# Kernel optimization log

Hardware: AMD Instinct MI355X
Metric: run time of the kernel (lower is better)

The kernel has to match this reference:

```python
import jax, jax.numpy as jnp
import numpy as np

D = 512          # embedding_dim (cfg.hidden_size)
K = 1024         # codebook_size
DECAY = 0.99
EPS = 1e-05
COMMITMENT_COST = 0.25


def setup_inputs() -> dict:
    key = jax.random.key(0)
    k1, k2, k3 = jax.random.split(key, 3)
    return {
        "inputs": jax.random.normal(k1, (32, 1024, D), dtype=jnp.float32),
        "embedding_weight": jax.random.normal(k2, (K, D), dtype=jnp.float32),
        "ema_cluster_size": jnp.zeros((K,), dtype=jnp.float32),
        "ema_w": jax.random.normal(k3, (K, D), dtype=jnp.float32),
    }


def reference(inputs, embedding_weight, ema_cluster_size, ema_w):
    input_shape = inputs.shape
    flat = inputs.reshape(-1, D)  # [N, D]

    # Squared L2 distances to every codebook entry: [N, K]
    distances = (
        jnp.sum(flat ** 2, axis=1, keepdims=True)
        + jnp.sum(embedding_weight ** 2, axis=1)
        - 2.0 * flat @ embedding_weight.T
    )
    idx = jnp.argmin(distances, axis=1)                      # [N]
    encodings = jax.nn.one_hot(idx, K, dtype=flat.dtype)     # [N, K]

    # ---- EMA codebook update (training path) ----
    counts = jnp.sum(encodings, axis=0)                      # == bincount(idx)
    new_cs = ema_cluster_size * DECAY + (1.0 - DECAY) * counts
    n = jnp.sum(new_cs)
    new_cs = (new_cs + EPS) / (n + K * EPS) * n              # Laplace smoothing
    # dw = encodings.T @ flat, done as a fused gather-reduce instead of dense matmul
    dw = jax.ops.segment_sum(flat, idx, num_segments=K)      # [K, D]
    new_ema_w = ema_w * DECAY + (1.0 - DECAY) * dw
    new_embedding = new_ema_w / new_cs[:, None]              # updated codebook

    # quantized = encodings @ new_embedding, expressed as a gather
    quantized = new_embedding[idx].reshape(input_shape)

    e_latent_loss = jnp.mean((jax.lax.stop_gradient(quantized) - inputs) ** 2)
    loss = COMMITMENT_COST * e_latent_loss

    # straight-through estimator
    quantized = inputs + jax.lax.stop_gradient(quantized - inputs)

    avg_probs = jnp.mean(encodings, axis=0)
    perplexity = jnp.exp(-jnp.sum(avg_probs * jnp.log(avg_probs + 1e-10)))
    return (loss, quantized, perplexity, encodings)
```

## Files before the change

### kernel.cpp

```cpp
#include <hip/hip_runtime.h>

#define NROWS 32768
#define DIM   512
#define KC    1024

typedef __attribute__((ext_vector_type(8)))  short short8v;
typedef __attribute__((ext_vector_type(16))) float f32x16;

#define AS1 __attribute__((address_space(1)))
#define AS3 __attribute__((address_space(3)))

__device__ __forceinline__ void split_bf16(float v, short& hi, short& lo) {
    unsigned u = __float_as_uint(v);
    unsigned r = u + 0x7FFFu + ((u >> 16) & 1u);
    hi = (short)(r >> 16);
    float hif = __uint_as_float(r & 0xFFFF0000u);
    float rem = v - hif;
    unsigned u2 = __float_as_uint(rem);
    unsigned r2 = u2 + 0x7FFFu + ((u2 >> 16) & 1u);
    lo = (short)(r2 >> 16);
}

__device__ __forceinline__ void conv8(const float4 a, const float4 b,
                                      short8v& hi, short8v& lo) {
    short h, l;
    split_bf16(a.x, h, l); hi[0] = h; lo[0] = l;
    split_bf16(a.y, h, l); hi[1] = h; lo[1] = l;
    split_bf16(a.z, h, l); hi[2] = h; lo[2] = l;
    split_bf16(a.w, h, l); hi[3] = h; lo[3] = l;
    split_bf16(b.x, h, l); hi[4] = h; lo[4] = l;
    split_bf16(b.y, h, l); hi[5] = h; lo[5] = l;
    split_bf16(b.z, h, l); hi[6] = h; lo[6] = l;
    split_bf16(b.w, h, l); hi[7] = h; lo[7] = l;
}

__device__ __forceinline__ unsigned long long pack_key(float d, int c) {
    unsigned u = __float_as_uint(d);
    u = (u & 0x80000000u) ? ~u : (u | 0x80000000u);
    return ((unsigned long long)u << 32) | (unsigned)c;
}

__global__ __launch_bounds__(256) void k_eprep(const float* __restrict__ E,
                                               short* __restrict__ efrag,
                                               float* __restrict__ en2,
                                               int* __restrict__ counts,
                                               unsigned long long* __restrict__ packed) {
    __shared__ short hbuf[32][520];
    __shared__ short lbuf[32][520];
    int b = blockIdx.x, t = threadIdx.x;
    const float* src = E + (size_t)b * 32 * DIM;
    short* dst = efrag + (size_t)b * 32768;

    unsigned long long* p = packed + b * 1024;
    #pragma unroll
    for (int i = 0; i < 4; ++i) p[t + i * 256] = 0xFFFFFFFFFFFFFFFFull;
    if (b == 0) {
        #pragma unroll
        for (int i = 0; i < 4; ++i) counts[t + i * 256] = 0;
    }

    #pragma unroll
    for (int f = 0; f < 16; ++f) {
        int u = t + f * 256;
        int row = u >> 7, c4 = (u & 127) * 4;
        float4 v = *reinterpret_cast<const float4*>(&src[row * DIM + c4]);
        short4 h4, l4;
        split_bf16(v.x, h4.x, l4.x); split_bf16(v.y, h4.y, l4.y);
        split_bf16(v.z, h4.z, l4.z); split_bf16(v.w, h4.w, l4.w);
        *reinterpret_cast<short4*>(&hbuf[row][c4]) = h4;
        *reinterpret_cast<short4*>(&lbuf[row][c4]) = l4;
    }
    __syncthreads();
    #pragma unroll
    for (int f = 0; f < 16; ++f) {
        int u = t + f * 256;
        int lane = u & 63, h = (u >> 6) & 1, kb = u >> 7;
        int row = lane & 31, k0 = kb * 16 + (lane >> 5) * 8;
        const short* s = h ? &lbuf[row][k0] : &hbuf[row][k0];
        short8v val = *reinterpret_cast<const short8v*>(s);
        *reinterpret_cast<short8v*>(&dst[(size_t)u * 8]) = val;
    }

    int w = t >> 6, lane = t & 63;
    for (int cc = 0; cc < 8; ++cc) {
        int c = b * 32 + w * 8 + cc;
        const float* row = E + (size_t)c * DIM;
        float4 a = *reinterpret_cast<const float4*>(&row[lane * 8]);
        float4 bb = *reinterpret_cast<const float4*>(&row[lane * 8 + 4]);
        float s = a.x*a.x + a.y*a.y + a.z*a.z + a.w*a.w
                + bb.x*bb.x + bb.y*bb.y + bb.z*bb.z + bb.w*bb.w;
        #pragma unroll
        for (int off = 32; off; off >>= 1) s += __shfl_xor(s, off);
        if (!lane) en2[c] = s;
    }
}

__global__ __launch_bounds__(256, 2) void k_argmin(const float* __restrict__ x,
                                                   const short* __restrict__ efrag,
                                                   const float* __restrict__ en2,
                                                   unsigned long long* __restrict__ packed) {
    __shared__ short sbuf[3][12288];
    const int tid = threadIdx.x;
    const int w = tid >> 6, l = tid & 63;
    const int wr = w >> 1, wc = w & 1;
    const int l31 = l & 31, lh = l >> 5;

    int bid = blockIdx.x;
    int xcd = bid & 7, j = bid >> 3;
    int row0 = (xcd * 32 + (j >> 2)) * 128;
    int c0   = (j & 3) * 256;

    const float* axsrc = x + (size_t)(row0 + w * 32 + l31) * DIM + lh * 8;
    const short* gsrc[4];
    #pragma unroll
    for (int s = 0; s < 4; ++s) {
        int gb = w * 2 + (s >> 1), h = s & 1;
        gsrc[s] = efrag + (size_t)(c0 / 32 + gb) * 32768 + h * 512 + l * 8;
    }

    f32x16 acc[2][4];
    #pragma unroll
    for (int a = 0; a < 2; ++a)
        #pragma unroll
        for (int b = 0; b < 4; ++b)
            #pragma unroll
            for (int r = 0; r < 16; ++r) acc[a][b][r] = 0.f;

    float4 a00 = *reinterpret_cast<const float4*>(axsrc);
    float4 a01 = *reinterpret_cast<const float4*>(axsrc + 4);
    __builtin_amdgcn_sched_barrier(0);
    #pragma unroll
    for (int s = 0; s < 4; ++s)
        __builtin_amdgcn_global_load_lds((const AS1 void*)gsrc[s],
                                         (AS3 void*)&sbuf[0][(8 + w * 4 + s) * 512],
                                         16, 0, 0);
    __builtin_amdgcn_sched_barrier(0);
    float4 a10 = *reinterpret_cast<const float4*>(axsrc + 16);
    float4 a11 = *reinterpret_cast<const float4*>(axsrc + 20);
    __builtin_amdgcn_sched_barrier(0);
    #pragma unroll
    for (int s = 0; s < 4; ++s)
        __builtin_amdgcn_global_load_lds((const AS1 void*)(gsrc[s] + 1024),
                                         (AS3 void*)&sbuf[1][(8 + w * 4 + s) * 512],
                                         16, 0, 0);
    {
        asm volatile("s_waitcnt vmcnt(10)" ::: "memory");
        short8v hi, lo; conv8(a00, a01, hi, lo);
        *reinterpret_cast<short8v*>(&sbuf[0][(w * 2 + 0) * 512 + l * 8]) = hi;
        *reinterpret_cast<short8v*>(&sbuf[0][(w * 2 + 1) * 512 + l * 8]) = lo;
        asm volatile("s_waitcnt vmcnt(4)" ::: "memory");
        conv8(a10, a11, hi, lo);
        *reinterpret_cast<short8v*>(&sbuf[1][(w * 2 + 0) * 512 + l * 8]) = hi;
        *reinterpret_cast<short8v*>(&sbuf[1][(w * 2 + 1) * 512 + l * 8]) = lo;
        asm volatile("s_waitcnt lgkmcnt(0)" ::: "memory");
        __builtin_amdgcn_s_barrier();
    }

    #pragma unroll 3
    for (int kb = 0; kb < 30; ++kb) {
        const int cur = kb % 3, nxt = (kb + 2) % 3;
        float4 an0 = *reinterpret_cast<const float4*>(axsrc + (kb + 2) * 16);
        float4 an1 = *reinterpret_cast<const float4*>(axsrc + (kb + 2) * 16 + 4);
        __builtin_amdgcn_sched_barrier(0);
        #pragma unroll
        for (int s = 0; s < 4; ++s)
            __builtin_amdgcn_global_load_lds(
                (const AS1 void*)(gsrc[s] + (size_t)(kb + 2) * 1024),
                (AS3 void*)&sbuf[nxt][(8 + w * 4 + s) * 512], 16, 0, 0);
        {
            short8v ah[2], al[2], bh[4], bl[4];
            const short* sb = sbuf[cur];
            #pragma unroll
            for (int m = 0; m < 2; ++m) {
                int g = wr * 2 + m;
                ah[m] = *reinterpret_cast<const short8v*>(&sb[(g * 2 + 0) * 512 + l * 8]);
                al[m] = *reinterpret_cast<const short8v*>(&sb[(g * 2 + 1) * 512 + l * 8]);
            }
            #pragma unroll
            for (int n = 0; n < 4; ++n) {
                int g = 4 + wc * 4 + n;
                bh[n] = *reinterpret_cast<const short8v*>(&sb[(g * 2 + 0) * 512 + l * 8]);
                bl[n] = *reinterpret_cast<const short8v*>(&sb[(g * 2 + 1) * 512 + l * 8]);
            }
            #pragma unroll
            for (int m = 0; m < 2; ++m)
                #pragma unroll
                for (int n = 0; n < 4; ++n) {
                    acc[m][n] = __builtin_amdgcn_mfma_f32_32x32x16_bf16(
                        ah[m], bh[n], acc[m][n], 0, 0, 0);
                    acc[m][n] = __builtin_amdgcn_mfma_f32_32x32x16_bf16(
                        ah[m], bl[n], acc[m][n], 0, 0, 0);
                    acc[m][n] = __builtin_amdgcn_mfma_f32_32x32x16_bf16(
                        al[m], bh[n], acc[m][n], 0, 0, 0);
                }
        }
        asm volatile("s_waitcnt vmcnt(4)" ::: "memory");
        {
            short8v hi, lo; conv8(an0, an1, hi, lo);
            *reinterpret_cast<short8v*>(&sbuf[nxt][(w * 2 + 0) * 512 + l * 8]) = hi;
            *reinterpret_cast<short8v*>(&sbuf[nxt][(w * 2 + 1) * 512 + l * 8]) = lo;
        }
        asm volatile("s_waitcnt lgkmcnt(0)" ::: "memory");
        __builtin_amdgcn_s_barrier();
    }

    #pragma unroll
    for (int e = 0; e < 2; ++e) {
        const int kb = 30 + e, cur = kb % 3;
        short8v ah[2], al[2], bh[4], bl[4];
        const short* sb = sbuf[cur];
        #pragma unroll
        for (int m = 0; m < 2; ++m) {
            int g = wr * 2 + m;
            ah[m] = *reinterpret_cast<const short8v*>(&sb[(g * 2 + 0) * 512 + l * 8]);
            al[m] = *reinterpret_cast<const short8v*>(&sb[(g * 2 + 1) * 512 + l * 8]);
        }
        #pragma unroll
        for (int n = 0; n < 4; ++n) {
            int g = 4 + wc * 4 + n;
            bh[n] = *reinterpret_cast<const short8v*>(&sb[(g * 2 + 0) * 512 + l * 8]);
            bl[n] = *reinterpret_cast<const short8v*>(&sb[(g * 2 + 1) * 512 + l * 8]);
        }
        #pragma unroll
        for (int m = 0; m < 2; ++m)
            #pragma unroll
            for (int n = 0; n < 4; ++n) {
                acc[m][n] = __builtin_amdgcn_mfma_f32_32x32x16_bf16(
                    ah[m], bh[n], acc[m][n], 0, 0, 0);
                acc[m][n] = __builtin_amdgcn_mfma_f32_32x32x16_bf16(
                    ah[m], bl[n], acc[m][n], 0, 0, 0);
                acc[m][n] = __builtin_amdgcn_mfma_f32_32x32x16_bf16(
                    al[m], bh[n], acc[m][n], 0, 0, 0);
            }
        if (e == 0) {
            asm volatile("s_waitcnt vmcnt(0) lgkmcnt(0)" ::: "memory");
            __builtin_amdgcn_s_barrier();
        }
    }

    float e2[4];
    #pragma unroll
    for (int n = 0; n < 4; ++n) e2[n] = en2[c0 + wc * 128 + n * 32 + l31];
    #pragma unroll
    for (int m = 0; m < 2; ++m) {
        #pragma unroll
        for (int r = 0; r < 16; ++r) {
            unsigned long long key = 0xFFFFFFFFFFFFFFFFull;
            #pragma unroll
            for (int n = 0; n < 4; ++n) {
                float d = fmaf(-2.f, acc[m][n][r], e2[n]);
                unsigned long long k = pack_key(d, c0 + wc * 128 + n * 32 + l31);
                if (k < key) key = k;
            }
            #pragma unroll
            for (int off = 1; off < 32; off <<= 1) {
                unsigned long long o = __shfl_xor(key, off);
                if (o < key) key = o;
            }
            if (l31 == 0) {
                int grow = row0 + wr * 64 + m * 32 + (r & 3) + 8 * (r >> 2) + 4 * lh;
                atomicMin(&packed[grow], key);
            }
        }
    }
}

__global__ __launch_bounds__(256) void k_hist(const unsigned long long* __restrict__ packed,
                                              int* __restrict__ idx,
                                              int* __restrict__ counts) {
    __shared__ int h[KC];
    for (int i = threadIdx.x; i < KC; i += 256) h[i] = 0;
    __syncthreads();
    int g = blockIdx.x * 256 + threadIdx.x;
    int c = (int)(unsigned)(packed[g] & 0xFFFFFFFFull);
    idx[g] = c;
    atomicAdd(&h[c], 1);
    __syncthreads();
    for (int i = threadIdx.x; i < KC; i += 256)
        if (h[i]) atomicAdd(&counts[i], h[i]);
}

__global__ __launch_bounds__(1024) void k_meta(const int* __restrict__ counts,
                                               const float* __restrict__ ema_cs,
                                               float* __restrict__ smoothed,
                                               int* __restrict__ offsets,
                                               int* __restrict__ cursor,
                                               float* __restrict__ perp_out) {
    __shared__ float ws1[16], ws2[16];
    __shared__ int wsum[16];
    int t = threadIdx.x, lane = t & 63, w = t >> 6;
    int cnt = counts[t];
    float cs = ema_cs[t] * 0.99f + 0.01f * (float)cnt;
    float p = (float)cnt / 32768.f;
    float v1 = cs, v2 = p * logf(p + 1e-10f);
    #pragma unroll
    for (int off = 32; off; off >>= 1) {
        v1 += __shfl_xor(v1, off);
        v2 += __shfl_xor(v2, off);
    }
    int s = cnt;
    #pragma unroll
    for (int off = 1; off < 64; off <<= 1) {
        int u = __shfl_up(s, off);
        if (lane >= off) s += u;
    }
    if (lane == 0) { ws1[w] = v1; ws2[w] = v2; }
    if (lane == 63) wsum[w] = s;
    __syncthreads();
    float n = 0.f;
    #pragma unroll
    for (int i = 0; i < 16; ++i) n += ws1[i];
    smoothed[t] = (cs + 1e-5f) / (n + 1024.f * 1e-5f) * n;
    if (t == 0) {
        float sp = 0.f;
        #pragma unroll
        for (int i = 0; i < 16; ++i) sp += ws2[i];
        perp_out[0] = expf(-sp);
    }
    int wo = 0;
    for (int i = 0; i < 16; ++i) if (i < w) wo += wsum[i];
    int off_ = wo + s - cnt;
    offsets[t] = off_;
    cursor[t] = off_;
}

__global__ __launch_bounds__(256) void k_scatter(const int* __restrict__ idx,
                                                 int* __restrict__ cursor,
                                                 int* __restrict__ bucket) {
    int g = blockIdx.x * 256 + threadIdx.x;
    int c = idx[g];
    int pos = atomicAdd(&cursor[c], 1);
    bucket[pos] = g;
}

__global__ __launch_bounds__(256) void k_dw(const float* __restrict__ x,
                                            const float* __restrict__ ema_w,
                                            const int* __restrict__ offsets,
                                            const int* __restrict__ counts,
                                            const int* __restrict__ bucket,
                                            const float* __restrict__ smoothed,
                                            float* __restrict__ newE) {
    __shared__ int rows[256];
    int k = blockIdx.x >> 1, half = blockIdx.x & 1, t = threadIdx.x;
    int d = half * 256 + t;
    int beg = offsets[k], m = counts[k];
    float a = 0.f;
    for (int base = 0; base < m; base += 256) {
        int n = min(256, m - base);
        __syncthreads();
        if (t < n) rows[t] = bucket[beg + base + t];
        __syncthreads();
        int i = 0;
        for (; i + 4 <= n; i += 4) {
            float v0 = x[(size_t)rows[i]     * DIM + d];
            float v1 = x[(size_t)rows[i + 1] * DIM + d];
            float v2 = x[(size_t)rows[i + 2] * DIM + d];
            float v3 = x[(size_t)rows[i + 3] * DIM + d];
            a += v0 + v1 + v2 + v3;
        }
        for (; i < n; ++i) a += x[(size_t)rows[i] * DIM + d];
    }
    newE[(size_t)k * DIM + d] =
        (ema_w[(size_t)k * DIM + d] * 0.99f + 0.01f * a) / smoothed[k];
}

__global__ __launch_bounds__(256) void k_qe(const float* __restrict__ x,
                                            const int* __restrict__ idx,
                                            const float* __restrict__ newE,
                                            float* __restrict__ outq,
                                            float* __restrict__ enc,
                                            float* __restrict__ partials) {
    int b = blockIdx.x, t = threadIdx.x;
    int row8 = b * 8;
    float lp = 0.f;
    #pragma unroll
    for (int it = 0; it < 4; ++it) {
        int slot = t + it * 256;
        int r = slot >> 7;
        int c4 = (slot & 127) * 4;
        int row = row8 + r;
        int code = idx[row];
        float4 in = *reinterpret_cast<const float4*>(&x[(size_t)row * DIM + c4]);
        float4 q  = *reinterpret_cast<const float4*>(&newE[(size_t)code * DIM + c4]);
        float4 d;
        d.x = q.x - in.x; d.y = q.y - in.y; d.z = q.z - in.z; d.w = q.w - in.w;
        float4 o;
        o.x = in.x + d.x; o.y = in.y + d.y; o.z = in.z + d.z; o.w = in.w + d.w;
        *reinterpret_cast<float4*>(&outq[(size_t)row * DIM + c4]) = o;
        lp += d.x*d.x + d.y*d.y + d.z*d.z + d.w*d.w;
    }
    {
        int er = row8 + (t >> 5);
        int l32 = t & 31;
        int one = idx[er];
        float4* dst = reinterpret_cast<float4*>(enc + (size_t)er * KC);
        #pragma unroll
        for (int s = 0; s < 8; ++s) {
            int c4 = l32 + s * 32;
            int base = c4 * 4;
            float4 v;
            v.x = (one == base)     ? 1.f : 0.f;
            v.y = (one == base + 1) ? 1.f : 0.f;
            v.z = (one == base + 2) ? 1.f : 0.f;
            v.w = (one == base + 3) ? 1.f : 0.f;
            dst[c4] = v;
        }
    }
    #pragma unroll
    for (int off = 32; off; off >>= 1) lp += __shfl_xor(lp, off);
    __shared__ float wr[4];
    int lane = t & 63, w = t >> 6;
    if (!lane) wr[w] = lp;
    __syncthreads();
    if (t == 0) partials[b] = wr[0] + wr[1] + wr[2] + wr[3];
}

__global__ __launch_bounds__(256) void k_lossfin(const float* __restrict__ partials,
                                                 float* __restrict__ out0) {
    __shared__ double red[256];
    double s = 0.0;
    for (int i = threadIdx.x; i < 4096; i += 256) s += (double)partials[i];
    red[threadIdx.x] = s; __syncthreads();
    for (int st = 128; st; st >>= 1) {
        if (threadIdx.x < st) red[threadIdx.x] += red[threadIdx.x + st];
        __syncthreads();
    }
    if (!threadIdx.x) out0[0] = (float)(0.25 * red[0] / 16777216.0);
}

extern "C" void kernel_launch(void* const* d_in, const int* in_sizes, int n_in,
                              void* d_out, int out_size, void* d_ws, size_t ws_size,
                              hipStream_t stream) {
    const float* x   = (const float*)d_in[0];
    const float* E   = (const float*)d_in[1];
    const float* ecs = (const float*)d_in[2];
    const float* emw = (const float*)d_in[3];
    float* out = (float*)d_out;

    char* ws = (char*)d_ws;
    int*   idx      = (int*)(ws + 0);
    int*   bucket   = (int*)(ws + 131072);
    float* en2      = (float*)(ws + 262144);
    int*   counts   = (int*)(ws + 266240);
    int*   offsets  = (int*)(ws + 270336);
    int*   cursor   = (int*)(ws + 274432);
    float* smoothed = (float*)(ws + 278528);
    float* newE     = (float*)(ws + 282624);
    float* partials = (float*)(ws + 282624 + 2097152);
    unsigned long long* packed = (unsigned long long*)newE;

    float* out_loss = out;
    float* out_q    = out + 1;
    float* out_perp = out + 16777217;
    float* out_enc  = out + 16777218;

    short* efrag = (short*)out_enc;

    k_eprep  <<<KC / 32, 256, 0, stream>>>(E, efrag, en2, counts, packed);
    k_argmin <<<(NROWS / 128) * 4, 256, 0, stream>>>(x, efrag, en2, packed);
    k_hist   <<<NROWS / 256, 256, 0, stream>>>(packed, idx, counts);
    k_meta   <<<1, 1024, 0, stream>>>(counts, ecs, smoothed, offsets, cursor, out_perp);
    k_scatter<<<NROWS / 256, 256, 0, stream>>>(idx, cursor, bucket);
    k_dw     <<<KC * 2, 256, 0, stream>>>(x, emw, offsets, counts, bucket, smoothed, newE);
    k_qe     <<<NROWS / 8, 256, 0, stream>>>(x, idx, newE, out_q, out_enc, partials);
    k_lossfin<<<1, 256, 0, stream>>>(partials, out_loss);
}
```

Baseline: 292.4 us.

## Make argmin GEMM wave-private: per-wave LDS B buffers, A in registers, no barriers

Restructures the k_argmin main loop so each wave keeps its own A fragments (hi/lo bf16 split) in registers and stages only its own B codebook tiles in a private double-buffered LDS region. This removes the block-wide s_barrier per k-step and the shared A staging through LDS. The cost is that each wave now loads 4 B tiles redundantly with the other row-wave, doubling global and LDS traffic for B. It also waits on vmcnt(0) every iteration, which gives only one stage of prefetch depth.

```diff
diff --git a/kernel.cpp b/kernel.cpp
--- a/kernel.cpp
+++ b/kernel.cpp
@@ -99,7 +99,7 @@
                                                    const short* __restrict__ efrag,
                                                    const float* __restrict__ en2,
                                                    unsigned long long* __restrict__ packed) {
-    __shared__ short sbuf[3][12288];
+    __shared__ short sbuf[4][2][8][512];
     const int tid = threadIdx.x;
     const int w = tid >> 6, l = tid & 63;
     const int wr = w >> 1, wc = w & 1;
@@ -110,13 +110,14 @@
     int row0 = (xcd * 32 + (j >> 2)) * 128;
     int c0   = (j & 3) * 256;
 
-    const float* axsrc = x + (size_t)(row0 + w * 32 + l31) * DIM + lh * 8;
+    const float* axsrc[2];
+    #pragma unroll
+    for (int m = 0; m < 2; ++m)
+        axsrc[m] = x + (size_t)(row0 + wr * 64 + m * 32 + l31) * DIM + lh * 8;
     const short* gsrc[4];
     #pragma unroll
-    for (int s = 0; s < 4; ++s) {
-        int gb = w * 2 + (s >> 1), h = s & 1;
-        gsrc[s] = efrag + (size_t)(c0 / 32 + gb) * 32768 + h * 512 + l * 8;
-    }
+    for (int n = 0; n < 4; ++n)
+        gsrc[n] = efrag + (size_t)(c0 / 32 + wc * 4 + n) * 32768 + l * 8;
 
     f32x16 acc[2][4];
     #pragma unroll
@@ -126,117 +127,77 @@
             #pragma unroll
             for (int r = 0; r < 16; ++r) acc[a][b][r] = 0.f;
 
-    float4 a00 = *reinterpret_cast<const float4*>(axsrc);
-    float4 a01 = *reinterpret_cast<const float4*>(axsrc + 4);
-    __builtin_amdgcn_sched_barrier(0);
-    #pragma unroll
-    for (int s = 0; s < 4; ++s)
-        __builtin_amdgcn_global_load_lds((const AS1 void*)gsrc[s],
-                                         (AS3 void*)&sbuf[0][(8 + w * 4 + s) * 512],
-                                         16, 0, 0);
-    __builtin_amdgcn_sched_barrier(0);
-    float4 a10 = *reinterpret_cast<const float4*>(axsrc + 16);
-    float4 a11 = *reinterpret_cast<const float4*>(axsrc + 20);
-    __builtin_amdgcn_sched_barrier(0);
-    #pragma unroll
-    for (int s = 0; s < 4; ++s)
-        __builtin_amdgcn_global_load_lds((const AS1 void*)(gsrc[s] + 1024),
-                                         (AS3 void*)&sbuf[1][(8 + w * 4 + s) * 512],
-                                         16, 0, 0);
+    short8v ah0[2], al0[2], ah1[2], al1[2];
+
     {
-        asm volatile("s_waitcnt vmcnt(10)" ::: "memory");
-        short8v hi, lo; conv8(a00, a01, hi, lo);
-        *reinterpret_cast<short8v*>(&sbuf[0][(w * 2 + 0) * 512 + l * 8]) = hi;
-        *reinterpret_cast<short8v*>(&sbuf[0][(w * 2 + 1) * 512 + l * 8]) = lo;
-        asm volatile("s_waitcnt vmcnt(4)" ::: "memory");
-        conv8(a10, a11, hi, lo);
-        *reinterpret_cast<short8v*>(&sbuf[1][(w * 2 + 0) * 512 + l * 8]) = hi;
-        *reinterpret_cast<short8v*>(&sbuf[1][(w * 2 + 1) * 512 + l * 8]) = lo;
-        asm volatile("s_waitcnt lgkmcnt(0)" ::: "memory");
-        __builtin_amdgcn_s_barrier();
-    }
-
-    #pragma unroll 3
-    for (int kb = 0; kb < 30; ++kb) {
-        const int cur = kb % 3, nxt = (kb + 2) % 3;
-        float4 an0 = *reinterpret_cast<const float4*>(axsrc + (kb + 2) * 16);
-        float4 an1 = *reinterpret_cast<const float4*>(axsrc + (kb + 2) * 16 + 4);
-        __builtin_amdgcn_sched_barrier(0);
-        #pragma unroll
-        for (int s = 0; s < 4; ++s)
-            __builtin_amdgcn_global_load_lds(
-                (const AS1 void*)(gsrc[s] + (size_t)(kb + 2) * 1024),
-                (AS3 void*)&sbuf[nxt][(8 + w * 4 + s) * 512], 16, 0, 0);
-        {
-            short8v ah[2], al[2], bh[4], bl[4];
-            const short* sb = sbuf[cur];
-            #pragma unroll
-            for (int m = 0; m < 2; ++m) {
-                int g = wr * 2 + m;
-                ah[m] = *reinterpret_cast<const short8v*>(&sb[(g * 2 + 0) * 512 + l * 8]);
-                al[m] = *reinterpret_cast<const short8v*>(&sb[(g * 2 + 1) * 512 + l * 8]);
-            }
-            #pragma unroll
-            for (int n = 0; n < 4; ++n) {
-                int g = 4 + wc * 4 + n;
-                bh[n] = *reinterpret_cast<const short8v*>(&sb[(g * 2 + 0) * 512 + l * 8]);
-                bl[n] = *reinterpret_cast<const short8v*>(&sb[(g * 2 + 1) * 512 + l * 8]);
-            }
-            #pragma unroll
-            for (int m = 0; m < 2; ++m)
-                #pragma unroll
-                for (int n = 0; n < 4; ++n) {
-                    acc[m][n] = __builtin_amdgcn_mfma_f32_32x32x16_bf16(
-                        ah[m], bh[n], acc[m][n], 0, 0, 0);
-                    acc[m][n] = __builtin_amdgcn_mfma_f32_32x32x16_bf16(
-                        ah[m], bl[n], acc[m][n], 0, 0, 0);
-                    acc[m][n] = __builtin_amdgcn_mfma_f32_32x32x16_bf16(
-                        al[m], bh[n], acc[m][n], 0, 0, 0);
-                }
+        float4 p0[2], p1[2];
+        #pragma unroll
+        for (int m = 0; m < 2; ++m) {
+            p0[m] = *reinterpret_cast<const float4*>(axsrc[m]);
+            p1[m] = *reinterpret_cast<const float4*>(axsrc[m] + 4);
         }
-        asm volatile("s_waitcnt vmcnt(4)" ::: "memory");
-        {
-            short8v hi, lo; conv8(an0, an1, hi, lo);
-            *reinterpret_cast<short8v*>(&sbuf[nxt][(w * 2 + 0) * 512 + l * 8]) = hi;
-            *reinterpret_cast<short8v*>(&sbuf[nxt][(w * 2 + 1) * 512 + l * 8]) = lo;
+        #pragma unroll
+        for (int n = 0; n < 4; ++n) {
+            __builtin_amdgcn_global_load_lds((const AS1 void*)gsrc[n],
+                                             (AS3 void*)&sbuf[w][0][n * 2 + 0][0], 16, 0, 0);
+            __builtin_amdgcn_global_load_lds((const AS1 void*)(gsrc[n] + 512),
+                                             (AS3 void*)&sbuf[w][0][n * 2 + 1][0], 16, 0, 0);
         }
-        asm volatile("s_waitcnt lgkmcnt(0)" ::: "memory");
-        __builtin_amdgcn_s_barrier();
-    }
-
-    #pragma unroll
-    for (int e = 0; e < 2; ++e) {
-        const int kb = 30 + e, cur = kb % 3;
-        short8v ah[2], al[2], bh[4], bl[4];
-        const short* sb = sbuf[cur];
-        #pragma unroll
-        for (int m = 0; m < 2; ++m) {
-            int g = wr * 2 + m;
-            ah[m] = *reinterpret_cast<const short8v*>(&sb[(g * 2 + 0) * 512 + l * 8]);
-            al[m] = *reinterpret_cast<const short8v*>(&sb[(g * 2 + 1) * 512 + l * 8]);
-        }
-        #pragma unroll
-        for (int n = 0; n < 4; ++n) {
-            int g = 4 + wc * 4 + n;
-            bh[n] = *reinterpret_cast<const short8v*>(&sb[(g * 2 + 0) * 512 + l * 8]);
-            bl[n] = *reinterpret_cast<const short8v*>(&sb[(g * 2 + 1) * 512 + l * 8]);
-        }
-        #pragma unroll
-        for (int m = 0; m < 2; ++m)
-            #pragma unroll
-            for (int n = 0; n < 4; ++n) {
-                acc[m][n] = __builtin_amdgcn_mfma_f32_32x32x16_bf16(
-                    ah[m], bh[n], acc[m][n], 0, 0, 0);
-                acc[m][n] = __builtin_amdgcn_mfma_f32_32x32x16_bf16(
-                    ah[m], bl[n], acc[m][n], 0, 0, 0);
-                acc[m][n] = __builtin_amdgcn_mfma_f32_32x32x16_bf16(
-                    al[m], bh[n], acc[m][n], 0, 0, 0);
-            }
-        if (e == 0) {
-            asm volatile("s_waitcnt vmcnt(0) lgkmcnt(0)" ::: "memory");
-            __builtin_amdgcn_s_barrier();
-        }
-    }
+        conv8(p0[0], p1[0], ah0[0], al0[0]);
+        conv8(p0[1], p1[1], ah0[1], al0[1]);
+    }
+
+#define KITER(KB, AHC, ALC, AHN, ALN, CUR, NXT, PREF)                          \
+    {                                                                          \
+        asm volatile("s_waitcnt vmcnt(0)" ::: "memory");                       \
+        float4 r0[2], r1[2];                                                   \
+        if (PREF) {                                                            \
+            _Pragma("unroll")                                                  \
+            for (int m = 0; m < 2; ++m) {                                      \
+                r0[m] = *reinterpret_cast<const float4*>(axsrc[m] + ((KB) + 1) * 16);     \
+                r1[m] = *reinterpret_cast<const float4*>(axsrc[m] + ((KB) + 1) * 16 + 4); \
+            }                                                                  \
+            _Pragma("unroll")                                                  \
+            for (int n = 0; n < 4; ++n) {                                      \
+                __builtin_amdgcn_global_load_lds(                              \
+                    (const AS1 void*)(gsrc[n] + (size_t)((KB) + 1) * 1024),    \
+                    (AS3 void*)&sbuf[w][NXT][n * 2 + 0][0], 16, 0, 0);         \
+                __builtin_amdgcn_global_load_lds(                              \
+                    (const AS1 void*)(gsrc[n] + (size_t)((KB) + 1) * 1024 + 512), \
+                    (AS3 void*)&sbuf[w][NXT][n * 2 + 1][0], 16, 0, 0);         \
+            }                                                                  \
+        }                                                                      \
+        short8v bh[4], bl[4];                                                  \
+        _Pragma("unroll")                                                      \
+        for (int n = 0; n < 4; ++n) {                                          \
+            bh[n] = *reinterpret_cast<const short8v*>(&sbuf[w][CUR][n * 2 + 0][l * 8]); \
+            bl[n] = *reinterpret_cast<const short8v*>(&sbuf[w][CUR][n * 2 + 1][l * 8]); \
+        }                                                                      \
+        _Pragma("unroll")                                                      \
+        for (int m = 0; m < 2; ++m) {                                          \
+            _Pragma("unroll")                                                  \
+            for (int n = 0; n < 4; ++n) {                                      \
+                acc[m][n] = __builtin_amdgcn_mfma_f32_32x32x16_bf16(AHC[m], bh[n], acc[m][n], 0, 0, 0); \
+                acc[m][n] = __builtin_amdgcn_mfma_f32_32x32x16_bf16(AHC[m], bl[n], acc[m][n], 0, 0, 0); \
+                acc[m][n] = __builtin_amdgcn_mfma_f32_32x32x16_bf16(ALC[m], bh[n], acc[m][n], 0, 0, 0); \
+            }                                                                  \
+        }                                                                      \
+        if (PREF) {                                                            \
+            conv8(r0[0], r1[0], AHN[0], ALN[0]);                               \
+            conv8(r0[1], r1[1], AHN[1], ALN[1]);                               \
+        }                                                                      \
+    }
+
+    for (int kp = 0; kp < 14; ++kp) {
+        const int kbe = kp * 2, kbo = kp * 2 + 1;
+        KITER(kbe, ah0, al0, ah1, al1, 0, 1, 1);
+        KITER(kbo, ah1, al1, ah0, al0, 1, 0, 1);
+    }
+    KITER(28, ah0, al0, ah1, al1, 0, 1, 1);
+    KITER(29, ah1, al1, ah0, al0, 1, 0, 1);
+    KITER(30, ah0, al0, ah1, al1, 0, 1, 1);
+    KITER(31, ah1, al1, ah0, al0, 1, 0, 0);
+#undef KITER
 
     float e2[4];
     #pragma unroll
```

After: 312.5 us. +6.9%, slower.

## Split segment-sum across sub-blocks with atomic accumulation and reorder MFMA chains

Applied to the files above, without the earlier changes.

The per-code gather-reduce for dw is split across 16 sub-blocks per code/half, with each accumulating into a zeroed fp32 buffer via atomicAdd. A separate finalize kernel then applies the EMA update and smoothing. This targets load imbalance when some codes receive many rows, at the cost of a larger grid, atomics, an extra zeroing pass and an extra launch. The MFMA loops are also reordered so the three product passes run as independent chains across accumulators rather than back-to-back on the same accumulator, which reduces dependency stalls.

```diff
diff --git a/kernel.cpp b/kernel.cpp
--- a/kernel.cpp
+++ b/kernel.cpp
@@ -44,7 +44,8 @@
                                                short* __restrict__ efrag,
                                                float* __restrict__ en2,
                                                int* __restrict__ counts,
-                                               unsigned long long* __restrict__ packed) {
+                                               unsigned long long* __restrict__ packed,
+                                               float* __restrict__ accb) {
     __shared__ short hbuf[32][520];
     __shared__ short lbuf[32][520];
     int b = blockIdx.x, t = threadIdx.x;
@@ -57,6 +58,11 @@
     if (b == 0) {
         #pragma unroll
         for (int i = 0; i < 4; ++i) counts[t + i * 256] = 0;
+    }
+    {
+        float* az = accb + (size_t)b * 16384;
+        #pragma unroll
+        for (int i = 0; i < 64; ++i) az[t + i * 256] = 0.f;
     }
 
     #pragma unroll
@@ -185,14 +191,21 @@
             #pragma unroll
             for (int m = 0; m < 2; ++m)
                 #pragma unroll
-                for (int n = 0; n < 4; ++n) {
+                for (int n = 0; n < 4; ++n)
                     acc[m][n] = __builtin_amdgcn_mfma_f32_32x32x16_bf16(
                         ah[m], bh[n], acc[m][n], 0, 0, 0);
+            #pragma unroll
+            for (int m = 0; m < 2; ++m)
+                #pragma unroll
+                for (int n = 0; n < 4; ++n)
                     acc[m][n] = __builtin_amdgcn_mfma_f32_32x32x16_bf16(
                         ah[m], bl[n], acc[m][n], 0, 0, 0);
+            #pragma unroll
+            for (int m = 0; m < 2; ++m)
+                #pragma unroll
+                for (int n = 0; n < 4; ++n)
                     acc[m][n] = __builtin_amdgcn_mfma_f32_32x32x16_bf16(
                         al[m], bh[n], acc[m][n], 0, 0, 0);
-                }
         }
         asm volatile("s_waitcnt vmcnt(4)" ::: "memory");
         {
@@ -224,14 +237,21 @@
         #pragma unroll
         for (int m = 0; m < 2; ++m)
             #pragma unroll
-            for (int n = 0; n < 4; ++n) {
+            for (int n = 0; n < 4; ++n)
                 acc[m][n] = __builtin_amdgcn_mfma_f32_32x32x16_bf16(
                     ah[m], bh[n], acc[m][n], 0, 0, 0);
+        #pragma unroll
+        for (int m = 0; m < 2; ++m)
+            #pragma unroll
+            for (int n = 0; n < 4; ++n)
                 acc[m][n] = __builtin_amdgcn_mfma_f32_32x32x16_bf16(
                     ah[m], bl[n], acc[m][n], 0, 0, 0);
+        #pragma unroll
+        for (int m = 0; m < 2; ++m)
+            #pragma unroll
+            for (int n = 0; n < 4; ++n)
                 acc[m][n] = __builtin_amdgcn_mfma_f32_32x32x16_bf16(
                     al[m], bh[n], acc[m][n], 0, 0, 0);
-            }
         if (e == 0) {
             asm volatile("s_waitcnt vmcnt(0) lgkmcnt(0)" ::: "memory");
             __builtin_amdgcn_s_barrier();
@@ -333,19 +353,20 @@
     bucket[pos] = g;
 }
 
-__global__ __launch_bounds__(256) void k_dw(const float* __restrict__ x,
-                                            const float* __restrict__ ema_w,
-                                            const int* __restrict__ offsets,
-                                            const int* __restrict__ counts,
-                                            const int* __restrict__ bucket,
-                                            const float* __restrict__ smoothed,
-                                            float* __restrict__ newE) {
+__global__ __launch_bounds__(256) void k_dwacc(const float* __restrict__ x,
+                                               const int* __restrict__ offsets,
+                                               const int* __restrict__ counts,
+                                               const int* __restrict__ bucket,
+                                               float* __restrict__ accb) {
     __shared__ int rows[256];
-    int k = blockIdx.x >> 1, half = blockIdx.x & 1, t = threadIdx.x;
+    int bid = blockIdx.x;
+    int k = bid >> 5, half = (bid >> 4) & 1, sub = bid & 15;
+    int t = threadIdx.x;
     int d = half * 256 + t;
     int beg = offsets[k], m = counts[k];
+    if (sub * 256 >= m) return;
     float a = 0.f;
-    for (int base = 0; base < m; base += 256) {
+    for (int base = sub * 256; base < m; base += 4096) {
         int n = min(256, m - base);
         __syncthreads();
         if (t < n) rows[t] = bucket[beg + base + t];
@@ -360,8 +381,16 @@
         }
         for (; i < n; ++i) a += x[(size_t)rows[i] * DIM + d];
     }
-    newE[(size_t)k * DIM + d] =
-        (ema_w[(size_t)k * DIM + d] * 0.99f + 0.01f * a) / smoothed[k];
+    atomicAdd(&accb[(size_t)k * DIM + d], a);
+}
+
+__global__ __launch_bounds__(256) void k_fin(const float* __restrict__ accb,
+                                             const float* __restrict__ ema_w,
+                                             const float* __restrict__ smoothed,
+                                             float* __restrict__ newE) {
+    int g = blockIdx.x * 256 + threadIdx.x;
+    int k = g >> 9;
+    newE[g] = (ema_w[g] * 0.99f + 0.01f * accb[g]) / smoothed[k];
 }
 
 __global__ __launch_bounds__(256) void k_qe(const float* __restrict__ x,
@@ -455,13 +484,15 @@
     float* out_enc  = out + 16777218;
 
     short* efrag = (short*)out_enc;
-
-    k_eprep  <<<KC / 32, 256, 0, stream>>>(E, efrag, en2, counts, packed);
+    float* accb  = (float*)(out_enc + 524288);
+
+    k_eprep  <<<KC / 32, 256, 0, stream>>>(E, efrag, en2, counts, packed, accb);
     k_argmin <<<(NROWS / 128) * 4, 256, 0, stream>>>(x, efrag, en2, packed);
     k_hist   <<<NROWS / 256, 256, 0, stream>>>(packed, idx, counts);
     k_meta   <<<1, 1024, 0, stream>>>(counts, ecs, smoothed, offsets, cursor, out_perp);
     k_scatter<<<NROWS / 256, 256, 0, stream>>>(idx, cursor, bucket);
-    k_dw     <<<KC * 2, 256, 0, stream>>>(x, emw, offsets, counts, bucket, smoothed, newE);
+    k_dwacc  <<<KC * 32, 256, 0, stream>>>(x, offsets, counts, bucket, accb);
+    k_fin    <<<2048, 256, 0, stream>>>(accb, emw, smoothed, newE);
     k_qe     <<<NROWS / 8, 256, 0, stream>>>(x, idx, newE, out_q, out_enc, partials);
     k_lossfin<<<1, 256, 0, stream>>>(partials, out_loss);
 }
```

Measured after the change: 279.6 us (median of 2 runs). 1.05x faster.
